# Kernel tuning notes

Hardware: AMD Instinct MI355X
Metric: run time of the kernel (lower is better)

The kernel has to match this reference:

```python
import jax, jax.numpy as jnp
import numpy as np

HEADS = 4
HID = 128
NEG_SLOPE = 0.2  # PyG GATConv default leaky_relu slope
EPS = 1e-16      # PyG softmax denominator epsilon


def _gat_layer(x, src, dst, W, att_src, att_dst, bias, N):
    # x: [N, F_in]; W: [F_in, HEADS*HID]; att_*: [HEADS, HID]; bias: [HID]
    h = (x @ W).reshape(N, HEADS, HID)                 # [N, H, C]
    a_s = jnp.sum(h * att_src[None], axis=-1)          # [N, H]
    a_d = jnp.sum(h * att_dst[None], axis=-1)          # [N, H]
    alpha = jax.nn.leaky_relu(a_s[src] + a_d[dst], NEG_SLOPE)  # [E, H]
    # segment softmax over edges grouped by destination node
    amax = jax.ops.segment_max(alpha, dst, num_segments=N)     # [N, H]
    ex = jnp.exp(alpha - amax[dst])                             # [E, H]
    denom = jax.ops.segment_sum(ex, dst, num_segments=N)       # [N, H]
    alpha = ex / (denom[dst] + EPS)
    msg = h[src] * alpha[:, :, None]                            # [E, H, C]
    out = jax.ops.segment_sum(msg, dst, num_segments=N)        # [N, H, C]
    return out.mean(axis=1) + bias                              # concat=False -> mean over heads


def setup_inputs() -> dict:
    key = jax.random.key(0)
    ks = jax.random.split(key, 12)
    N, E, F_in = 50000, 400000, 256
    x = jax.random.normal(ks[0], (N, F_in), dtype=jnp.float32)
    edge_index = jax.random.randint(ks[1], (2, E), 0, N, dtype=jnp.int64)
    s1 = 1.0 / np.sqrt(F_in)
    s2 = 1.0 / np.sqrt(HID)
    return {
        "x": x,
        "edge_index": edge_index,
        "W1": jax.random.normal(ks[2], (F_in, HEADS * HID), dtype=jnp.float32) * s1,
        "att_src1": jax.random.normal(ks[3], (HEADS, HID), dtype=jnp.float32) * s2,
        "att_dst1": jax.random.normal(ks[4], (HEADS, HID), dtype=jnp.float32) * s2,
        "b1": jnp.zeros((HID,), dtype=jnp.float32),
        "W2": jax.random.normal(ks[5], (HID, HEADS * HID), dtype=jnp.float32) * s2,
        "att_src2": jax.random.normal(ks[6], (HEADS, HID), dtype=jnp.float32) * s2,
        "att_dst2": jax.random.normal(ks[7], (HEADS, HID), dtype=jnp.float32) * s2,
        "b2": jnp.zeros((HID,), dtype=jnp.float32),
    }


def reference(x, edge_index, W1, att_src1, att_dst1, b1, W2, att_src2, att_dst2, b2):
    N = x.shape[0]
    # PyG GATConv default add_self_loops=True
    loop = jnp.arange(N, dtype=edge_index.dtype)
    src = jnp.concatenate([edge_index[0], loop])
    dst = jnp.concatenate([edge_index[1], loop])
    h = jax.nn.relu(_gat_layer(x, src, dst, W1, att_src1, att_dst1, b1, N))
    h = jax.nn.relu(_gat_layer(h, src, dst, W2, att_src2, att_dst2, b2, N))
    # dropout is identity in eval mode
    return h
```

## Files before the change

kernel.cpp:

```cpp
#include <hip/hip_runtime.h>
#include <hip/hip_bf16.h>
#include <cstdint>

#define HEADS 4
#define HID 128
#define F_OUT 512
#define NEG_SLOPE 0.2f
#define GAT_EPS 1e-16f

typedef __attribute__((ext_vector_type(8))) short bf16x8;
typedef __attribute__((ext_vector_type(4))) float f32x4;

__device__ __forceinline__ float bf2f(unsigned short u) {
  unsigned int x = ((unsigned int)u) << 16;
  return __builtin_bit_cast(float, x);
}
__device__ __forceinline__ unsigned short f2b(float f) {
  unsigned int u = __builtin_bit_cast(unsigned int, f);
  unsigned int r = (u + 0x7fffu + ((u >> 16) & 1u)) >> 16;
  return (unsigned short)r;
}

__global__ __launch_bounds__(256) void detect_i64_kernel(const unsigned int* __restrict__ e,
                                                         int* __restrict__ flag) {
  __shared__ int nz;
  if (threadIdx.x == 0) nz = 0;
  __syncthreads();
  for (int i = threadIdx.x; i < 2048; i += blockDim.x) {
    if (e[2 * i + 1] != 0u) atomicOr(&nz, 1);
  }
  __syncthreads();
  if (threadIdx.x == 0) *flag = (nz == 0) ? 1 : 0;
}

__device__ __forceinline__ int edge_at(const int* __restrict__ e32,
                                       const long long* __restrict__ e64,
                                       int f, int i) {
  return f ? (int)e64[i] : e32[i];
}

__global__ __launch_bounds__(256) void hist_kernel(const int* __restrict__ e32,
                                                   const long long* __restrict__ e64,
                                                   const int* __restrict__ flag,
                                                   int* __restrict__ counts, int E, int N) {
  int i = blockIdx.x * 256 + threadIdx.x;
  int total = E + N;
  if (i >= total) return;
  int f = *flag;
  int dst = (i < E) ? edge_at(e32, e64, f, E + i) : (i - E);
  atomicAdd(&counts[dst], 1);
}

__global__ __launch_bounds__(256) void scan_partial_kernel(const int* __restrict__ counts,
                                                           int* __restrict__ partials, int N) {
  int t = threadIdx.x;
  int lane = t & 63, wv = t >> 6;
  int idx = blockIdx.x * 1024 + t * 4;
  int4 v = make_int4(0, 0, 0, 0);
  if (idx + 3 < N) v = *(const int4*)&counts[idx];
  else {
    if (idx + 0 < N) v.x = counts[idx + 0];
    if (idx + 1 < N) v.y = counts[idx + 1];
    if (idx + 2 < N) v.z = counts[idx + 2];
  }
  int s = v.x + v.y + v.z + v.w;
#pragma unroll
  for (int off = 32; off > 0; off >>= 1) s += __shfl_xor(s, off);
  __shared__ int wsum[4];
  if (lane == 0) wsum[wv] = s;
  __syncthreads();
  if (t == 0) partials[blockIdx.x] = wsum[0] + wsum[1] + wsum[2] + wsum[3];
}

__global__ __launch_bounds__(256) void scan_base_kernel(int* __restrict__ partials,
                                                        int* __restrict__ offsets,
                                                        int nblocks, int N) {
  __shared__ int buf[1024];
  int t = threadIdx.x;
  for (int i = t; i < nblocks; i += 256) buf[i] = partials[i];
  __syncthreads();
  if (t == 0) {
    int run = 0;
    for (int i = 0; i < nblocks; i++) { int c = buf[i]; buf[i] = run; run += c; }
    offsets[N] = run;
  }
  __syncthreads();
  for (int i = t; i < nblocks; i += 256) partials[i] = buf[i];
}

__global__ __launch_bounds__(256) void scan_final_kernel(const int* __restrict__ counts,
                                                         const int* __restrict__ partials,
                                                         int* __restrict__ offsets,
                                                         int* __restrict__ cursor, int N) {
  int t = threadIdx.x;
  int lane = t & 63, wv = t >> 6;
  int idx = blockIdx.x * 1024 + t * 4;
  int4 v = make_int4(0, 0, 0, 0);
  if (idx + 3 < N) v = *(const int4*)&counts[idx];
  else {
    if (idx + 0 < N) v.x = counts[idx + 0];
    if (idx + 1 < N) v.y = counts[idx + 1];
    if (idx + 2 < N) v.z = counts[idx + 2];
  }
  int s1 = v.x, s2 = s1 + v.y, s3 = s2 + v.z, s4 = s3 + v.w;
  int val = s4;
#pragma unroll
  for (int off = 1; off < 64; off <<= 1) {
    int y = __shfl_up(val, off);
    if (lane >= off) val += y;
  }
  __shared__ int wsum[4];
  if (lane == 63) wsum[wv] = val;
  __syncthreads();
  int wbase = 0;
  for (int i = 0; i < wv; i++) wbase += wsum[i];
  int excl = partials[blockIdx.x] + wbase + (val - s4);
  if (idx + 0 < N) { offsets[idx + 0] = excl;      cursor[idx + 0] = excl; }
  if (idx + 1 < N) { offsets[idx + 1] = excl + s1; cursor[idx + 1] = excl + s1; }
  if (idx + 2 < N) { offsets[idx + 2] = excl + s2; cursor[idx + 2] = excl + s2; }
  if (idx + 3 < N) { offsets[idx + 3] = excl + s3; cursor[idx + 3] = excl + s3; }
}

__global__ __launch_bounds__(256) void scatter_kernel(const int* __restrict__ e32,
                                                      const long long* __restrict__ e64,
                                                      const int* __restrict__ flag,
                                                      int* __restrict__ cursor,
                                                      int* __restrict__ csr_src, int E, int N) {
  int i = blockIdx.x * 256 + threadIdx.x;
  int total = E + N;
  if (i >= total) return;
  int f = *flag;
  int src, dst;
  if (i < E) { src = edge_at(e32, e64, f, i); dst = edge_at(e32, e64, f, E + i); }
  else       { src = i - E; dst = src; }
  int pos = atomicAdd(&cursor[dst], 1);
  csr_src[pos] = src;
}

__global__ __launch_bounds__(256) void cvt_w_kernel(const float* __restrict__ W,
                                                    unsigned short* __restrict__ Wt, int K) {
  int idx = blockIdx.x * 256 + threadIdx.x;
  if (idx >= K * F_OUT) return;
  int k = idx / F_OUT, c = idx % F_OUT;
  Wt[c * K + k] = f2b(W[idx]);
}

#define LDK 40
template <int AF32>
__global__ __launch_bounds__(256) void gemm_att_kernel(const void* __restrict__ Araw,
                                                       const unsigned short* __restrict__ Bt,
                                                       unsigned short* __restrict__ C,
                                                       const float* __restrict__ att_s,
                                                       const float* __restrict__ att_d,
                                                       float* __restrict__ a_s,
                                                       float* __restrict__ a_d,
                                                       int M, int K) {
  __shared__ unsigned short As[128][LDK];
  __shared__ unsigned short Bs[128][LDK];
  __shared__ float sred[2][128];
  __shared__ float dred[2][128];
  int tid = threadIdx.x;
  int lane = tid & 63, wid = tid >> 6;
  int wr = wid >> 1, wc = wid & 1;
  int head = blockIdx.y;
  int rowBase = blockIdx.x * 128, colBase = head * 128;
  f32x4 acc[4][4];
#pragma unroll
  for (int i = 0; i < 4; i++)
#pragma unroll
    for (int j = 0; j < 4; j++) acc[i][j] = (f32x4){0.f, 0.f, 0.f, 0.f};

  int fr = lane & 15, fk = (lane >> 4) * 8;

  for (int k0 = 0; k0 < K; k0 += 32) {
#pragma unroll
    for (int i = 0; i < 2; i++) {
      int idx = i * 256 + tid;
      int r = idx >> 2, cq = (idx & 3) * 8;
      int gr = rowBase + r;
      if (AF32) {
        const float* Af = (const float*)Araw;
        float4 v0 = make_float4(0.f, 0.f, 0.f, 0.f), v1 = v0;
        if (gr < M) {
          v0 = *(const float4*)&Af[(size_t)gr * K + k0 + cq];
          v1 = *(const float4*)&Af[(size_t)gr * K + k0 + cq + 4];
        }
        bf16x8 o;
        o[0] = (short)f2b(v0.x); o[1] = (short)f2b(v0.y);
        o[2] = (short)f2b(v0.z); o[3] = (short)f2b(v0.w);
        o[4] = (short)f2b(v1.x); o[5] = (short)f2b(v1.y);
        o[6] = (short)f2b(v1.z); o[7] = (short)f2b(v1.w);
        *(bf16x8*)&As[r][cq] = o;
      } else {
        const unsigned short* Ab = (const unsigned short*)Araw;
        float4 va = make_float4(0.f, 0.f, 0.f, 0.f);
        if (gr < M) va = *(const float4*)&Ab[(size_t)gr * K + k0 + cq];
        *(float4*)&As[r][cq] = va;
      }
      *(float4*)&Bs[r][cq] = *(const float4*)&Bt[(size_t)(colBase + r) * K + k0 + cq];
    }
    __syncthreads();
    bf16x8 af[4], bfv[4];
#pragma unroll
    for (int mi = 0; mi < 4; mi++)
      af[mi] = *(const bf16x8*)&As[wr * 64 + mi * 16 + fr][fk];
#pragma unroll
    for (int ni = 0; ni < 4; ni++)
      bfv[ni] = *(const bf16x8*)&Bs[wc * 64 + ni * 16 + fr][fk];
#pragma unroll
    for (int mi = 0; mi < 4; mi++)
#pragma unroll
      for (int ni = 0; ni < 4; ni++)
        acc[mi][ni] = __builtin_amdgcn_mfma_f32_16x16x32_bf16(af[mi], bfv[ni], acc[mi][ni], 0, 0, 0);
    __syncthreads();
  }

  int r0 = rowBase + wr * 64, c0 = colBase + wc * 64;
#pragma unroll
  for (int mi = 0; mi < 4; mi++) {
#pragma unroll
    for (int ni = 0; ni < 4; ni++) {
      int col = c0 + ni * 16 + (lane & 15);
#pragma unroll
      for (int q = 0; q < 4; q++) {
        int row = r0 + mi * 16 + (lane >> 4) * 4 + q;
        if (row < M) C[(size_t)row * F_OUT + col] = f2b(acc[mi][ni][q]);
      }
    }
  }

  float asv[4], adv[4];
#pragma unroll
  for (int ni = 0; ni < 4; ni++) {
    int cih = wc * 64 + ni * 16 + (lane & 15);
    asv[ni] = att_s[head * HID + cih];
    adv[ni] = att_d[head * HID + cih];
  }
#pragma unroll
  for (int mi = 0; mi < 4; mi++) {
#pragma unroll
    for (int q = 0; q < 4; q++) {
      float ps = 0.f, pd = 0.f;
#pragma unroll
      for (int ni = 0; ni < 4; ni++) {
        ps += acc[mi][ni][q] * asv[ni];
        pd += acc[mi][ni][q] * adv[ni];
      }
#pragma unroll
      for (int off = 1; off < 16; off <<= 1) {
        ps += __shfl_xor(ps, off);
        pd += __shfl_xor(pd, off);
      }
      if ((lane & 15) == 0) {
        int rl = wr * 64 + mi * 16 + (lane >> 4) * 4 + q;
        sred[wc][rl] = ps;
        dred[wc][rl] = pd;
      }
    }
  }
  __syncthreads();
  if (tid < 128) {
    int row = rowBase + tid;
    if (row < M) {
      a_s[row * HEADS + head] = sred[0][tid] + sred[1][tid];
      a_d[row * HEADS + head] = dred[0][tid] + dred[1][tid];
    }
  }
}

__global__ __launch_bounds__(256) void norm_kernel(const int* __restrict__ offsets,
                                                   const int* __restrict__ csr_src,
                                                   const float* __restrict__ a_s,
                                                   const float* __restrict__ a_d,
                                                   float* __restrict__ alpha, int N) {
  int t = blockIdx.x * 256 + threadIdx.x;
  if (t >= N * HEADS) return;
  int n = t >> 2, hh = t & 3;
  int beg = offsets[n], end = offsets[n + 1];
  float adn = a_d[n * HEADS + hh];
  float m = -1e30f;
  for (int i = beg; i < end; i++) {
    float al = a_s[csr_src[i] * HEADS + hh] + adn;
    al = (al > 0.f) ? al : al * NEG_SLOPE;
    alpha[i * HEADS + hh] = al;
    m = fmaxf(m, al);
  }
  float denom = 0.f;
  for (int i = beg; i < end; i++) {
    float ex = __expf(alpha[i * HEADS + hh] - m);
    alpha[i * HEADS + hh] = ex;
    denom += ex;
  }
  float inv = 1.f / (denom + GAT_EPS);
  for (int i = beg; i < end; i++) alpha[i * HEADS + hh] *= inv;
}

template <int OUT_BF>
__global__ __launch_bounds__(256) void aggregate_kernel(const unsigned short* __restrict__ h,
                                                        const float* __restrict__ wexp,
                                                        const int* __restrict__ offsets,
                                                        const int* __restrict__ csr_src,
                                                        const float* __restrict__ bias,
                                                        void* __restrict__ out, int N) {
  int n = blockIdx.x;
  int w = threadIdx.x >> 6;
  int lane = threadIdx.x & 63;
  int slot = lane >> 4, sl = lane & 15;
  int beg = offsets[n], end = offsets[n + 1];

  float acc[8];
#pragma unroll
  for (int j = 0; j < 8; j++) acc[j] = 0.f;

  int e = beg + slot;
  int s = 0; float wgt = 0.f;
  if (e < end) { s = csr_src[e]; wgt = wexp[e * HEADS + w]; }
  while (e < end) {
    int ne = e + 4;
    int ns = 0; float nw = 0.f;
    if (ne < end) { ns = csr_src[ne]; nw = wexp[ne * HEADS + w]; }
    bf16x8 hv = *(const bf16x8*)&h[(size_t)s * F_OUT + w * HID + sl * 8];
#pragma unroll
    for (int j = 0; j < 8; j++) acc[j] += bf2f((unsigned short)hv[j]) * wgt;
    e = ne; s = ns; wgt = nw;
  }
#pragma unroll
  for (int j = 0; j < 8; j++) {
    acc[j] += __shfl_xor(acc[j], 16);
    acc[j] += __shfl_xor(acc[j], 32);
  }

  __shared__ float red[HEADS][HID];
  if (slot == 0) {
#pragma unroll
    for (int j = 0; j < 8; j++) red[w][sl * 8 + j] = acc[j];
  }
  __syncthreads();
  if (threadIdx.x < HID) {
    int c = threadIdx.x;
    float v = (red[0][c] + red[1][c] + red[2][c] + red[3][c]) * 0.25f + bias[c];
    v = fmaxf(v, 0.f);
    if (OUT_BF)
      ((unsigned short*)out)[(size_t)n * HID + c] = f2b(v);
    else
      ((float*)out)[(size_t)n * HID + c] = v;
  }
}

extern "C" void kernel_launch(void* const* d_in, const int* in_sizes, int n_in,
                              void* d_out, int out_size, void* d_ws, size_t ws_size,
                              hipStream_t stream) {
  const float* x   = (const float*)d_in[0];
  const int* e32   = (const int*)d_in[1];
  const long long* e64 = (const long long*)d_in[1];
  const float* W1  = (const float*)d_in[2];
  const float* as1 = (const float*)d_in[3];
  const float* ad1 = (const float*)d_in[4];
  const float* b1  = (const float*)d_in[5];
  const float* W2  = (const float*)d_in[6];
  const float* as2 = (const float*)d_in[7];
  const float* ad2 = (const float*)d_in[8];
  const float* b2  = (const float*)d_in[9];

  int F_in = in_sizes[2] / F_OUT;
  int N = in_sizes[0] / F_in;
  int E = in_sizes[1] / 2;
  int Etot = E + N;

  char* ws = (char*)d_ws;
  size_t off = 0;
  auto alloc = [&](size_t bytes) -> void* {
    void* p = ws + off;
    off = (off + bytes + 255) & ~(size_t)255;
    return p;
  };
  unsigned short* h_bf   = (unsigned short*)alloc((size_t)N * F_OUT * 2);
  unsigned short* out1_bf= (unsigned short*)alloc((size_t)N * HID * 2);
  unsigned short* Wt1    = (unsigned short*)alloc((size_t)F_in * F_OUT * 2);
  unsigned short* Wt2    = (unsigned short*)alloc((size_t)HID * F_OUT * 2);
  float* a_s    = (float*)alloc((size_t)N * HEADS * 4);
  float* a_d    = (float*)alloc((size_t)N * HEADS * 4);
  float* alpha  = (float*)alloc((size_t)Etot * HEADS * 4);
  int* counts   = (int*)alloc((size_t)(N + 1) * 4);
  int* offsets  = (int*)alloc((size_t)(N + 1) * 4);
  int* cursor   = (int*)alloc((size_t)N * 4);
  int* csr_src  = (int*)alloc((size_t)Etot * 4);
  int* partials = (int*)alloc(1024 * 4);
  int* flag     = (int*)alloc(256);
  if (off > ws_size) return;

  int nchunks = (N + 1023) / 1024;

  hipMemsetAsync(counts, 0, (size_t)N * 4, stream);
  detect_i64_kernel<<<1, 256, 0, stream>>>((const unsigned int*)d_in[1], flag);
  hist_kernel<<<(Etot + 255) / 256, 256, 0, stream>>>(e32, e64, flag, counts, E, N);
  scan_partial_kernel<<<nchunks, 256, 0, stream>>>(counts, partials, N);
  scan_base_kernel<<<1, 256, 0, stream>>>(partials, offsets, nchunks, N);
  scan_final_kernel<<<nchunks, 256, 0, stream>>>(counts, partials, offsets, cursor, N);
  scatter_kernel<<<(Etot + 255) / 256, 256, 0, stream>>>(e32, e64, flag, cursor, csr_src, E, N);

  cvt_w_kernel<<<(F_in * F_OUT + 255) / 256, 256, 0, stream>>>(W1, Wt1, F_in);
  cvt_w_kernel<<<(HID * F_OUT + 255) / 256, 256, 0, stream>>>(W2, Wt2, HID);

  dim3 ggrid((N + 127) / 128, HEADS);
  int nblocks = (N * HEADS + 255) / 256;
  gemm_att_kernel<1><<<ggrid, 256, 0, stream>>>(x, Wt1, h_bf, as1, ad1, a_s, a_d, N, F_in);
  norm_kernel<<<nblocks, 256, 0, stream>>>(offsets, csr_src, a_s, a_d, alpha, N);
  aggregate_kernel<1><<<N, 256, 0, stream>>>(h_bf, alpha, offsets, csr_src, b1, out1_bf, N);
  gemm_att_kernel<0><<<ggrid, 256, 0, stream>>>(out1_bf, Wt2, h_bf, as2, ad2, a_s, a_d, N, HID);
  norm_kernel<<<nblocks, 256, 0, stream>>>(offsets, csr_src, a_s, a_d, alpha, N);
  aggregate_kernel<0><<<N, 256, 0, stream>>>(h_bf, alpha, offsets, csr_src, b2, d_out, N);
}
```

Before: 358.4 us.

## Drop softmax max pass, defer normalization to aggregate, prefetch two edges ahead

```diff
diff --git a/kernel.cpp b/kernel.cpp
--- a/kernel.cpp
+++ b/kernel.cpp
@@ -272,32 +272,28 @@
                                                    const int* __restrict__ csr_src,
                                                    const float* __restrict__ a_s,
                                                    const float* __restrict__ a_d,
-                                                   float* __restrict__ alpha, int N) {
+                                                   float* __restrict__ alpha,
+                                                   float* __restrict__ denom, int N) {
   int t = blockIdx.x * 256 + threadIdx.x;
   if (t >= N * HEADS) return;
   int n = t >> 2, hh = t & 3;
   int beg = offsets[n], end = offsets[n + 1];
   float adn = a_d[n * HEADS + hh];
-  float m = -1e30f;
+  float den = 0.f;
   for (int i = beg; i < end; i++) {
     float al = a_s[csr_src[i] * HEADS + hh] + adn;
     al = (al > 0.f) ? al : al * NEG_SLOPE;
-    alpha[i * HEADS + hh] = al;
-    m = fmaxf(m, al);
-  }
-  float denom = 0.f;
-  for (int i = beg; i < end; i++) {
-    float ex = __expf(alpha[i * HEADS + hh] - m);
+    float ex = __expf(al);
     alpha[i * HEADS + hh] = ex;
-    denom += ex;
-  }
-  float inv = 1.f / (denom + GAT_EPS);
-  for (int i = beg; i < end; i++) alpha[i * HEADS + hh] *= inv;
+    den += ex;
+  }
+  denom[t] = den;
 }
 
 template <int OUT_BF>
 __global__ __launch_bounds__(256) void aggregate_kernel(const unsigned short* __restrict__ h,
                                                         const float* __restrict__ wexp,
+                                                        const float* __restrict__ denom,
                                                         const int* __restrict__ offsets,
                                                         const int* __restrict__ csr_src,
                                                         const float* __restrict__ bias,
@@ -312,17 +308,32 @@
 #pragma unroll
   for (int j = 0; j < 8; j++) acc[j] = 0.f;
 
+  bf16x8 r0 = {}, r1 = {};
+  float w0 = 0.f, w1 = 0.f;
   int e = beg + slot;
-  int s = 0; float wgt = 0.f;
-  if (e < end) { s = csr_src[e]; wgt = wexp[e * HEADS + w]; }
-  while (e < end) {
-    int ne = e + 4;
-    int ns = 0; float nw = 0.f;
-    if (ne < end) { ns = csr_src[ne]; nw = wexp[ne * HEADS + w]; }
-    bf16x8 hv = *(const bf16x8*)&h[(size_t)s * F_OUT + w * HID + sl * 8];
-#pragma unroll
-    for (int j = 0; j < 8; j++) acc[j] += bf2f((unsigned short)hv[j]) * wgt;
-    e = ne; s = ns; wgt = nw;
+  if (e < end) {
+    int s = csr_src[e];
+    w0 = wexp[e * HEADS + w];
+    r0 = *(const bf16x8*)&h[(size_t)s * F_OUT + w * HID + sl * 8];
+  }
+  if (e + 4 < end) {
+    int s = csr_src[e + 4];
+    w1 = wexp[(e + 4) * HEADS + w];
+    r1 = *(const bf16x8*)&h[(size_t)s * F_OUT + w * HID + sl * 8];
+  }
+  for (; e < end; e += 4) {
+    bf16x8 rc = r0; float wc = w0;
+    r0 = r1; w0 = w1;
+    int en = e + 8;
+    if (en < end) {
+      int s = csr_src[en];
+      w1 = wexp[en * HEADS + w];
+      r1 = *(const bf16x8*)&h[(size_t)s * F_OUT + w * HID + sl * 8];
+    } else {
+      w1 = 0.f;
+    }
+#pragma unroll
+    for (int j = 0; j < 8; j++) acc[j] += bf2f((unsigned short)rc[j]) * wc;
   }
 #pragma unroll
   for (int j = 0; j < 8; j++) {
@@ -330,10 +341,11 @@
     acc[j] += __shfl_xor(acc[j], 32);
   }
 
+  float inv = 1.f / (denom[n * HEADS + w] + GAT_EPS);
   __shared__ float red[HEADS][HID];
   if (slot == 0) {
 #pragma unroll
-    for (int j = 0; j < 8; j++) red[w][sl * 8 + j] = acc[j];
+    for (int j = 0; j < 8; j++) red[w][sl * 8 + j] = acc[j] * inv;
   }
   __syncthreads();
   if (threadIdx.x < HID) {
@@ -380,6 +392,7 @@
   unsigned short* Wt2    = (unsigned short*)alloc((size_t)HID * F_OUT * 2);
   float* a_s    = (float*)alloc((size_t)N * HEADS * 4);
   float* a_d    = (float*)alloc((size_t)N * HEADS * 4);
+  float* denom  = (float*)alloc((size_t)N * HEADS * 4);
   float* alpha  = (float*)alloc((size_t)Etot * HEADS * 4);
   int* counts   = (int*)alloc((size_t)(N + 1) * 4);
   int* offsets  = (int*)alloc((size_t)(N + 1) * 4);
@@ -405,9 +418,9 @@
   dim3 ggrid((N + 127) / 128, HEADS);
   int nblocks = (N * HEADS + 255) / 256;
   gemm_att_kernel<1><<<ggrid, 256, 0, stream>>>(x, Wt1, h_bf, as1, ad1, a_s, a_d, N, F_in);
-  norm_kernel<<<nblocks, 256, 0, stream>>>(offsets, csr_src, a_s, a_d, alpha, N);
-  aggregate_kernel<1><<<N, 256, 0, stream>>>(h_bf, alpha, offsets, csr_src, b1, out1_bf, N);
+  norm_kernel<<<nblocks, 256, 0, stream>>>(offsets, csr_src, a_s, a_d, alpha, denom, N);
+  aggregate_kernel<1><<<N, 256, 0, stream>>>(h_bf, alpha, denom, offsets, csr_src, b1, out1_bf, N);
   gemm_att_kernel<0><<<ggrid, 256, 0, stream>>>(out1_bf, Wt2, h_bf, as2, ad2, a_s, a_d, N, HID);
-  norm_kernel<<<nblocks, 256, 0, stream>>>(offsets, csr_src, a_s, a_d, alpha, N);
-  aggregate_kernel<0><<<N, 256, 0, stream>>>(h_bf, alpha, offsets, csr_src, b2, d_out, N);
-}
+  norm_kernel<<<nblocks, 256, 0, stream>>>(offsets, csr_src, a_s, a_d, alpha, denom, N);
+  aggregate_kernel<0><<<N, 256, 0, stream>>>(h_bf, alpha, denom, offsets, csr_src, b2, d_out, N);
+}
```

Result: no change. 353.8 us (-1.3%).
